# Optimization experiments

Measured on AMD Instinct MI355X. Metric: run time of the kernel, lower is better.

The kernel has to match this reference:

```python
import jax, jax.numpy as jnp
import numpy as np

S = 4            # symbol_features (number of element types)
NLAB = S * S     # label_features = 16
RC = 6.0         # cutoff radius
C1, C2 = 32, 64  # embedding_layers
B, N = 4, 512
BOX_L = 25.0     # non-periodic box extent for coordinate sampling


def setup_inputs() -> dict:
    key = jax.random.key(0)
    k1, k2, k3, k4 = jax.random.split(key, 4)
    coords = jax.random.uniform(k1, (B, N, 3), dtype=jnp.float32) * BOX_L
    numbers = jax.random.randint(k2, (B, N), 0, S)
    # NaN lattice -> Descriptor takes the non-periodic neighbor branch
    boxs = jnp.full((B, 9), jnp.nan, dtype=jnp.float32)
    # RConv parameters (per label): nuww=-0.05, sigmas=4.0, centres ~ xavier_normal
    nuww0 = jnp.full((NLAB,), -0.05, jnp.float32)
    sigmas0 = jnp.full((NLAB,), 4.0, jnp.float32)
    centres0 = (jax.random.normal(k3, (NLAB, C1)) * np.sqrt(2.0 / (NLAB + C1))).astype(jnp.float32)
    nuww1 = jnp.full((NLAB,), -0.05, jnp.float32)
    sigmas1 = jnp.full((NLAB,), 4.0, jnp.float32)
    centres1 = (jax.random.normal(k4, (NLAB, C2)) * np.sqrt(2.0 / (NLAB + C2))).astype(jnp.float32)
    return {"boxs": boxs, "numbers": numbers, "coords": coords,
            "nuww0": nuww0, "sigmas0": sigmas0, "centres0": centres0,
            "nuww1": nuww1, "sigmas1": sigmas1, "centres1": centres1}


def _rconv(label, r, nuww, sigmas, centres):
    # label: [B,N,N] int; r: [B,N,N,Cin] -> out [B,N,N,Cout]
    rs = r.sum(-1, keepdims=True)            # sum over channel dim (keepdim)
    ww = nuww[label][..., None]              # [B,N,N,1]
    sgm = sigmas[label][..., None]           # [B,N,N,1]
    cc = centres[label]                      # [B,N,N,Cout]
    alpha = (rs - cc) * sgm
    return ww * jnp.exp(-(alpha * alpha))


def reference(boxs, numbers, coords, nuww0, sigmas0, centres0, nuww1, sigmas1, centres1):
    # boxs is NaN -> non-periodic branch of Descriptor.forward.
    # Dense-mask formulation: pairs (i,j) with d<=RC, i!=j; masked entries
    # contribute exactly zero to the per-atom contractions below.
    rij = coords[:, None, :, :] - coords[:, :, None, :]      # [B,N,N,3] = x_j - x_i
    d2 = jnp.sum(rij * rij, axis=-1)                         # [B,N,N]
    safe = jnp.sqrt(jnp.where(d2 > 0, d2, 1.0))              # NaN-safe sqrt for grads
    d = jnp.where(d2 > 0, safe, 0.0)
    eye = jnp.eye(N, dtype=bool)
    mask = (jax.lax.stop_gradient(d) <= RC) & ~eye           # neighbor list (detached, as in torch)

    fc = 0.5 * jnp.cos(d * (jnp.pi / RC)) + 0.5              # cutoff_cosine, [B,N,N]
    ang = rij / safe[..., None]                              # unit direction (safe at diag)
    raij = jnp.concatenate([fc[..., None], ang * fc[..., None]], axis=-1)  # [B,N,N,4]

    label = numbers[:, :, None] * S + numbers[:, None, :]    # ZIJ_Label[z_i, z_j], [B,N,N]

    r0 = fc[..., None]                                       # rij_cos, [B,N,N,1]
    phi = _rconv(label, r0, nuww0, sigmas0, centres0)        # [B,N,N,C1]
    phi = _rconv(label, phi, nuww1, sigmas1, centres1)       # [B,N,N,C2]
    phi = phi * mask[..., None]                              # zero out non-neighbors

    # per atom i: L = phi^T @ raij over neighbors j -> [C2,4]; R = L @ L^T -> [C2,C2]
    Lm = jnp.einsum('bijc,bijf->bicf', phi, raij)            # [B,N,C2,4]
    R = jnp.einsum('bicf,bidf->bicd', Lm, Lm)                # [B,N,C2,C2]
    fro = jnp.sqrt(jnp.sum(R * R, axis=(-2, -1), keepdims=True))
    D = R / fro
    return D.reshape(B, N, C2 * C2)                          # Dij [B,N,4096]
```

## Files before the change

### kernel.cpp

```cpp
#include <hip/hip_runtime.h>
#include <math.h>

#define S_ 4
#define NLAB 16
#define C1 32
#define C2 64
#define N_ 512
#define RC 6.0f
#define PI_OVER_RC 0.5235987755982988f
#define NBMAX 96

__global__ __launch_bounds__(256, 4) void desc_kernel(
    const int* __restrict__ numbers,
    const float* __restrict__ coords,
    const float* __restrict__ nuww0, const float* __restrict__ sigmas0,
    const float* __restrict__ centres0,
    const float* __restrict__ nuww1, const float* __restrict__ sigmas1,
    const float* __restrict__ centres1,
    float* __restrict__ out)
{
    __shared__ float s_c0[NLAB * 33];
    __shared__ float s_c1[NLAB * C2];
    __shared__ float s_ww0[NLAB], s_sg0[NLAB], s_ww1[NLAB], s_sg1[NLAB];
    __shared__ float4 s_pair[4][NBMAX];
    __shared__ float  s_s1[4][NBMAX];
    __shared__ int    s_lab[4][NBMAX];
    __shared__ float4 s_Lm[4][C2];

    const int tid  = threadIdx.x;
    const int w    = tid >> 6;
    const int lane = tid & 63;
    const int bi   = blockIdx.x * 4 + w;
    const int b    = bi >> 9;
    const int i    = bi & (N_ - 1);
    const int base = b * N_;

    for (int idx = tid; idx < NLAB * C1; idx += 256) {
        int l = idx >> 5, c = idx & 31;
        s_c0[l * 33 + c] = centres0[idx];
    }
    for (int idx = tid; idx < NLAB * C2; idx += 256) s_c1[idx] = centres1[idx];
    if (tid < NLAB) {
        s_ww0[tid] = nuww0[tid]; s_sg0[tid] = sigmas0[tid];
        s_ww1[tid] = nuww1[tid]; s_sg1[tid] = sigmas1[tid];
    }
    __syncthreads();

    const float xi = coords[(base + i) * 3 + 0];
    const float yi = coords[(base + i) * 3 + 1];
    const float zi = coords[(base + i) * 3 + 2];
    const int zlab = numbers[base + i] * S_;

    int cnt = 0;
    #pragma unroll
    for (int t = 0; t < 8; ++t) {
        int j = t * 64 + lane;
        float dx = coords[(base + j) * 3 + 0] - xi;
        float dy = coords[(base + j) * 3 + 1] - yi;
        float dz = coords[(base + j) * 3 + 2] - zi;
        float d2 = dx * dx + dy * dy + dz * dz;
        float d  = sqrtf(d2);
        bool hit = (j != i) && (d <= RC);
        unsigned long long m = __ballot(hit);
        int slot = cnt + __popcll(m & ((1ull << lane) - 1ull));
        if (hit && slot < NBMAX) {
            s_pair[w][slot] = make_float4(dx, dy, dz, d);
            s_lab[w][slot]  = zlab + numbers[base + j];
        }
        cnt += __popcll(m);
    }
    const int nn = min(cnt, NBMAX);
    __builtin_amdgcn_wave_barrier();

    for (int k = lane; k < nn; k += 64) {
        float4 g  = s_pair[w][k];
        int   lab = s_lab[w][k];
        float fc  = 0.5f * __cosf(g.w * PI_OVER_RC) + 0.5f;
        float sg0 = s_sg0[lab];
        const float* c0 = &s_c0[lab * 33];
        float p0 = 0.f, p1 = 0.f;
        #pragma unroll
        for (int c = 0; c < C1; c += 2) {
            float a0 = (fc - c0[c])     * sg0;
            float a1 = (fc - c0[c + 1]) * sg0;
            p0 += __expf(-(a0 * a0));
            p1 += __expf(-(a1 * a1));
        }
        float fac = (g.w > 0.f) ? (fc / g.w) : 0.f;
        s_pair[w][k] = make_float4(fc, g.x * fac, g.y * fac, g.z * fac);
        s_s1[w][k]   = s_ww0[lab] * (p0 + p1);
    }
    __builtin_amdgcn_wave_barrier();

    float a0 = 0.f, a1 = 0.f, a2 = 0.f, a3 = 0.f;
    for (int k = 0; k < nn; ++k) {
        int    lab = s_lab[w][k];
        float  s1  = s_s1[w][k];
        float4 r4  = s_pair[w][k];
        float  al  = (s1 - s_c1[lab * C2 + lane]) * s_sg1[lab];
        float  p   = s_ww1[lab] * __expf(-(al * al));
        a0 += p * r4.x; a1 += p * r4.y; a2 += p * r4.z; a3 += p * r4.w;
    }
    s_Lm[w][lane] = make_float4(a0, a1, a2, a3);
    __builtin_amdgcn_wave_barrier();

    float g00 = a0 * a0, g01 = a0 * a1, g02 = a0 * a2, g03 = a0 * a3;
    float g11 = a1 * a1, g12 = a1 * a2, g13 = a1 * a3;
    float g22 = a2 * a2, g23 = a2 * a3, g33 = a3 * a3;
    #pragma unroll
    for (int off = 32; off >= 1; off >>= 1) {
        g00 += __shfl_xor(g00, off, 64); g01 += __shfl_xor(g01, off, 64);
        g02 += __shfl_xor(g02, off, 64); g03 += __shfl_xor(g03, off, 64);
        g11 += __shfl_xor(g11, off, 64); g12 += __shfl_xor(g12, off, 64);
        g13 += __shfl_xor(g13, off, 64); g22 += __shfl_xor(g22, off, 64);
        g23 += __shfl_xor(g23, off, 64); g33 += __shfl_xor(g33, off, 64);
    }
    float ss = g00 * g00 + g11 * g11 + g22 * g22 + g33 * g33
             + 2.f * (g01 * g01 + g02 * g02 + g03 * g03
                    + g12 * g12 + g13 * g13 + g23 * g23);
    float inv = rsqrtf(ss);

    float4 Lc0_ = s_Lm[w][(lane & 15) * 4 + 0];
    float4 Lc1_ = s_Lm[w][(lane & 15) * 4 + 1];
    float4 Lc2_ = s_Lm[w][(lane & 15) * 4 + 2];
    float4 Lc3_ = s_Lm[w][(lane & 15) * 4 + 3];
    float* po = out + (size_t)bi * (C2 * C2);
    #pragma unroll
    for (int q = 0; q < 16; ++q) {
        int dd = q * 4 + (lane >> 4);
        float4 Ld = s_Lm[w][dd];
        float4 v;
        v.x = (Lc0_.x * Ld.x + Lc0_.y * Ld.y + Lc0_.z * Ld.z + Lc0_.w * Ld.w) * inv;
        v.y = (Lc1_.x * Ld.x + Lc1_.y * Ld.y + Lc1_.z * Ld.z + Lc1_.w * Ld.w) * inv;
        v.z = (Lc2_.x * Ld.x + Lc2_.y * Ld.y + Lc2_.z * Ld.z + Lc2_.w * Ld.w) * inv;
        v.w = (Lc3_.x * Ld.x + Lc3_.y * Ld.y + Lc3_.z * Ld.z + Lc3_.w * Ld.w) * inv;
        *reinterpret_cast<float4*>(po + q * 256 + lane * 4) = v;
    }
}

extern "C" void kernel_launch(void* const* d_in, const int* in_sizes, int n_in,
                              void* d_out, int out_size, void* d_ws, size_t ws_size,
                              hipStream_t stream) {
    const int*   numbers  = (const int*)  d_in[1];
    const float* coords   = (const float*)d_in[2];
    const float* nuww0    = (const float*)d_in[3];
    const float* sigmas0  = (const float*)d_in[4];
    const float* centres0 = (const float*)d_in[5];
    const float* nuww1    = (const float*)d_in[6];
    const float* sigmas1  = (const float*)d_in[7];
    const float* centres1 = (const float*)d_in[8];
    float* out = (float*)d_out;

    const int B = in_sizes[1] / N_;
    dim3 grid(B * N_ / 4), block(256);
    desc_kernel<<<grid, block, 0, stream>>>(numbers, coords, nuww0, sigmas0,
                                            centres0, nuww1, sigmas1, centres1, out);
}
```

Measured before the change: 19.43 us.

## Split descriptor into Lm kernel and separate outer-product store kernel

After: 23.54 us. +21.2%, slower.

```diff
diff --git a/kernel.cpp b/kernel.cpp
--- a/kernel.cpp
+++ b/kernel.cpp
@@ -10,14 +10,14 @@
 #define PI_OVER_RC 0.5235987755982988f
 #define NBMAX 96
 
-__global__ __launch_bounds__(256, 4) void desc_kernel(
+__global__ __launch_bounds__(256) void lm_kernel(
     const int* __restrict__ numbers,
     const float* __restrict__ coords,
     const float* __restrict__ nuww0, const float* __restrict__ sigmas0,
     const float* __restrict__ centres0,
     const float* __restrict__ nuww1, const float* __restrict__ sigmas1,
     const float* __restrict__ centres1,
-    float* __restrict__ out)
+    float4* __restrict__ ws)
 {
     __shared__ float s_c0[NLAB * 33];
     __shared__ float s_c1[NLAB * C2];
@@ -25,7 +25,6 @@
     __shared__ float4 s_pair[4][NBMAX];
     __shared__ float  s_s1[4][NBMAX];
     __shared__ int    s_lab[4][NBMAX];
-    __shared__ float4 s_Lm[4][C2];
 
     const int tid  = threadIdx.x;
     const int w    = tid >> 6;
@@ -101,8 +100,6 @@
         float  p   = s_ww1[lab] * __expf(-(al * al));
         a0 += p * r4.x; a1 += p * r4.y; a2 += p * r4.z; a3 += p * r4.w;
     }
-    s_Lm[w][lane] = make_float4(a0, a1, a2, a3);
-    __builtin_amdgcn_wave_barrier();
 
     float g00 = a0 * a0, g01 = a0 * a1, g02 = a0 * a2, g03 = a0 * a3;
     float g11 = a1 * a1, g12 = a1 * a2, g13 = a1 * a3;
@@ -118,23 +115,34 @@
     float ss = g00 * g00 + g11 * g11 + g22 * g22 + g33 * g33
              + 2.f * (g01 * g01 + g02 * g02 + g03 * g03
                     + g12 * g12 + g13 * g13 + g23 * g23);
-    float inv = rsqrtf(ss);
+    float sqinv = sqrtf(rsqrtf(ss));
 
-    float4 Lc0_ = s_Lm[w][(lane & 15) * 4 + 0];
-    float4 Lc1_ = s_Lm[w][(lane & 15) * 4 + 1];
-    float4 Lc2_ = s_Lm[w][(lane & 15) * 4 + 2];
-    float4 Lc3_ = s_Lm[w][(lane & 15) * 4 + 3];
+    ws[bi * C2 + lane] = make_float4(a0 * sqinv, a1 * sqinv, a2 * sqinv, a3 * sqinv);
+}
+
+__global__ __launch_bounds__(256, 8) void outer_kernel(
+    const float4* __restrict__ ws,
+    float* __restrict__ out)
+{
+    __shared__ float4 sL[C2];
+    const int tid = threadIdx.x;
+    const int bi  = blockIdx.x;
+
+    if (tid < C2) sL[tid] = ws[bi * C2 + tid];
+    __syncthreads();
+
+    const int cb = (tid & 15) * 4;
+    float4 Lc0 = sL[cb + 0], Lc1 = sL[cb + 1], Lc2 = sL[cb + 2], Lc3 = sL[cb + 3];
     float* po = out + (size_t)bi * (C2 * C2);
     #pragma unroll
-    for (int q = 0; q < 16; ++q) {
-        int dd = q * 4 + (lane >> 4);
-        float4 Ld = s_Lm[w][dd];
+    for (int q = 0; q < 4; ++q) {
+        float4 Ld = sL[q * 16 + (tid >> 4)];
         float4 v;
-        v.x = (Lc0_.x * Ld.x + Lc0_.y * Ld.y + Lc0_.z * Ld.z + Lc0_.w * Ld.w) * inv;
-        v.y = (Lc1_.x * Ld.x + Lc1_.y * Ld.y + Lc1_.z * Ld.z + Lc1_.w * Ld.w) * inv;
-        v.z = (Lc2_.x * Ld.x + Lc2_.y * Ld.y + Lc2_.z * Ld.z + Lc2_.w * Ld.w) * inv;
-        v.w = (Lc3_.x * Ld.x + Lc3_.y * Ld.y + Lc3_.z * Ld.z + Lc3_.w * Ld.w) * inv;
-        *reinterpret_cast<float4*>(po + q * 256 + lane * 4) = v;
+        v.x = Lc0.x * Ld.x + Lc0.y * Ld.y + Lc0.z * Ld.z + Lc0.w * Ld.w;
+        v.y = Lc1.x * Ld.x + Lc1.y * Ld.y + Lc1.z * Ld.z + Lc1.w * Ld.w;
+        v.z = Lc2.x * Ld.x + Lc2.y * Ld.y + Lc2.z * Ld.z + Lc2.w * Ld.w;
+        v.w = Lc3.x * Ld.x + Lc3.y * Ld.y + Lc3.z * Ld.z + Lc3.w * Ld.w;
+        *reinterpret_cast<float4*>(po + q * 1024 + tid * 4) = v;
     }
 }
 
@@ -150,9 +158,10 @@
     const float* sigmas1  = (const float*)d_in[7];
     const float* centres1 = (const float*)d_in[8];
     float* out = (float*)d_out;
+    float4* ws = (float4*)d_ws;
 
     const int B = in_sizes[1] / N_;
-    dim3 grid(B * N_ / 4), block(256);
-    desc_kernel<<<grid, block, 0, stream>>>(numbers, coords, nuww0, sigmas0,
-                                            centres0, nuww1, sigmas1, centres1, out);
+    lm_kernel<<<dim3(B * N_ / 4), dim3(256), 0, stream>>>(
+        numbers, coords, nuww0, sigmas0, centres0, nuww1, sigmas1, centres1, ws);
+    outer_kernel<<<dim3(B * N_), dim3(256), 0, stream>>>(ws, out);
 }
```

## Split each atom's neighbor work across four waves with shared-memory reduction

Applied to the files above, without the earlier changes.

New measurement: 22.28 us. 14.7% more time.

```diff
diff --git a/kernel.cpp b/kernel.cpp
--- a/kernel.cpp
+++ b/kernel.cpp
@@ -8,9 +8,9 @@
 #define N_ 512
 #define RC 6.0f
 #define PI_OVER_RC 0.5235987755982988f
-#define NBMAX 96
+#define SEGCAP 32
 
-__global__ __launch_bounds__(256, 4) void desc_kernel(
+__global__ __launch_bounds__(256, 8) void desc_kernel(
     const int* __restrict__ numbers,
     const float* __restrict__ coords,
     const float* __restrict__ nuww0, const float* __restrict__ sigmas0,
@@ -22,15 +22,16 @@
     __shared__ float s_c0[NLAB * 33];
     __shared__ float s_c1[NLAB * C2];
     __shared__ float s_ww0[NLAB], s_sg0[NLAB], s_ww1[NLAB], s_sg1[NLAB];
-    __shared__ float4 s_pair[4][NBMAX];
-    __shared__ float  s_s1[4][NBMAX];
-    __shared__ int    s_lab[4][NBMAX];
-    __shared__ float4 s_Lm[4][C2];
+    __shared__ float4 s_pair[4][SEGCAP];
+    __shared__ float  s_s1[4][SEGCAP];
+    __shared__ int    s_lab[4][SEGCAP];
+    __shared__ float4 s_part[4][C2];
+    __shared__ float4 s_Lm[C2];
 
     const int tid  = threadIdx.x;
-    const int w    = tid >> 6;
+    const int wq   = tid >> 6;
     const int lane = tid & 63;
-    const int bi   = blockIdx.x * 4 + w;
+    const int bi   = blockIdx.x;
     const int b    = bi >> 9;
     const int i    = bi & (N_ - 1);
     const int base = b * N_;
@@ -51,30 +52,32 @@
     const float zi = coords[(base + i) * 3 + 2];
     const int zlab = numbers[base + i] * S_;
 
-    int cnt = 0;
+    int cntq = 0;
     #pragma unroll
-    for (int t = 0; t < 8; ++t) {
-        int j = t * 64 + lane;
+    for (int t = 0; t < 2; ++t) {
+        int j = wq * 128 + t * 64 + lane;
         float dx = coords[(base + j) * 3 + 0] - xi;
         float dy = coords[(base + j) * 3 + 1] - yi;
         float dz = coords[(base + j) * 3 + 2] - zi;
+        int   zj = numbers[base + j];
         float d2 = dx * dx + dy * dy + dz * dz;
         float d  = sqrtf(d2);
         bool hit = (j != i) && (d <= RC);
         unsigned long long m = __ballot(hit);
-        int slot = cnt + __popcll(m & ((1ull << lane) - 1ull));
-        if (hit && slot < NBMAX) {
-            s_pair[w][slot] = make_float4(dx, dy, dz, d);
-            s_lab[w][slot]  = zlab + numbers[base + j];
+        int slot = cntq + __popcll(m & ((1ull << lane) - 1ull));
+        if (hit && slot < SEGCAP) {
+            s_pair[wq][slot] = make_float4(dx, dy, dz, d);
+            s_lab[wq][slot]  = zlab + zj;
         }
-        cnt += __popcll(m);
+        cntq += __popcll(m);
     }
-    const int nn = min(cnt, NBMAX);
+    const int nnq = min(cntq, SEGCAP);
     __builtin_amdgcn_wave_barrier();
 
-    for (int k = lane; k < nn; k += 64) {
-        float4 g  = s_pair[w][k];
-        int   lab = s_lab[w][k];
+    if (lane < nnq) {
+        int   k   = lane;
+        float4 g  = s_pair[wq][k];
+        int   lab = s_lab[wq][k];
         float fc  = 0.5f * __cosf(g.w * PI_OVER_RC) + 0.5f;
         float sg0 = s_sg0[lab];
         const float* c0 = &s_c0[lab * 33];
@@ -87,22 +90,32 @@
             p1 += __expf(-(a1 * a1));
         }
         float fac = (g.w > 0.f) ? (fc / g.w) : 0.f;
-        s_pair[w][k] = make_float4(fc, g.x * fac, g.y * fac, g.z * fac);
-        s_s1[w][k]   = s_ww0[lab] * (p0 + p1);
+        s_pair[wq][k] = make_float4(fc, g.x * fac, g.y * fac, g.z * fac);
+        s_s1[wq][k]   = s_ww0[lab] * (p0 + p1);
     }
     __builtin_amdgcn_wave_barrier();
 
-    float a0 = 0.f, a1 = 0.f, a2 = 0.f, a3 = 0.f;
-    for (int k = 0; k < nn; ++k) {
-        int    lab = s_lab[w][k];
-        float  s1  = s_s1[w][k];
-        float4 r4  = s_pair[w][k];
-        float  al  = (s1 - s_c1[lab * C2 + lane]) * s_sg1[lab];
-        float  p   = s_ww1[lab] * __expf(-(al * al));
-        a0 += p * r4.x; a1 += p * r4.y; a2 += p * r4.z; a3 += p * r4.w;
+    {
+        float a0 = 0.f, a1 = 0.f, a2 = 0.f, a3 = 0.f;
+        for (int k = 0; k < nnq; ++k) {
+            int    lab = s_lab[wq][k];
+            float  s1  = s_s1[wq][k];
+            float4 r4  = s_pair[wq][k];
+            float  al  = (s1 - s_c1[lab * C2 + lane]) * s_sg1[lab];
+            float  p   = s_ww1[lab] * __expf(-(al * al));
+            a0 += p * r4.x; a1 += p * r4.y; a2 += p * r4.z; a3 += p * r4.w;
+        }
+        s_part[wq][lane] = make_float4(a0, a1, a2, a3);
     }
-    s_Lm[w][lane] = make_float4(a0, a1, a2, a3);
-    __builtin_amdgcn_wave_barrier();
+    __syncthreads();
+
+    float4 P0 = s_part[0][lane], P1 = s_part[1][lane];
+    float4 P2 = s_part[2][lane], P3 = s_part[3][lane];
+    float a0 = (P0.x + P1.x) + (P2.x + P3.x);
+    float a1 = (P0.y + P1.y) + (P2.y + P3.y);
+    float a2 = (P0.z + P1.z) + (P2.z + P3.z);
+    float a3 = (P0.w + P1.w) + (P2.w + P3.w);
+    s_Lm[lane] = make_float4(a0, a1, a2, a3);
 
     float g00 = a0 * a0, g01 = a0 * a1, g02 = a0 * a2, g03 = a0 * a3;
     float g11 = a1 * a1, g12 = a1 * a2, g13 = a1 * a3;
@@ -119,21 +132,26 @@
              + 2.f * (g01 * g01 + g02 * g02 + g03 * g03
                     + g12 * g12 + g13 * g13 + g23 * g23);
     float inv = rsqrtf(ss);
+    __builtin_amdgcn_wave_barrier();
 
-    float4 Lc0_ = s_Lm[w][(lane & 15) * 4 + 0];
-    float4 Lc1_ = s_Lm[w][(lane & 15) * 4 + 1];
-    float4 Lc2_ = s_Lm[w][(lane & 15) * 4 + 2];
-    float4 Lc3_ = s_Lm[w][(lane & 15) * 4 + 3];
+    const int cb = (lane & 15) * 4;
+    float4 Lc0 = s_Lm[cb + 0], Lc1 = s_Lm[cb + 1];
+    float4 Lc2 = s_Lm[cb + 2], Lc3 = s_Lm[cb + 3];
+    Lc0.x *= inv; Lc0.y *= inv; Lc0.z *= inv; Lc0.w *= inv;
+    Lc1.x *= inv; Lc1.y *= inv; Lc1.z *= inv; Lc1.w *= inv;
+    Lc2.x *= inv; Lc2.y *= inv; Lc2.z *= inv; Lc2.w *= inv;
+    Lc3.x *= inv; Lc3.y *= inv; Lc3.z *= inv; Lc3.w *= inv;
     float* po = out + (size_t)bi * (C2 * C2);
     #pragma unroll
-    for (int q = 0; q < 16; ++q) {
+    for (int t = 0; t < 4; ++t) {
+        int q  = wq * 4 + t;
         int dd = q * 4 + (lane >> 4);
-        float4 Ld = s_Lm[w][dd];
+        float4 Ld = s_Lm[dd];
         float4 v;
-        v.x = (Lc0_.x * Ld.x + Lc0_.y * Ld.y + Lc0_.z * Ld.z + Lc0_.w * Ld.w) * inv;
-        v.y = (Lc1_.x * Ld.x + Lc1_.y * Ld.y + Lc1_.z * Ld.z + Lc1_.w * Ld.w) * inv;
-        v.z = (Lc2_.x * Ld.x + Lc2_.y * Ld.y + Lc2_.z * Ld.z + Lc2_.w * Ld.w) * inv;
-        v.w = (Lc3_.x * Ld.x + Lc3_.y * Ld.y + Lc3_.z * Ld.z + Lc3_.w * Ld.w) * inv;
+        v.x = Lc0.x * Ld.x + Lc0.y * Ld.y + Lc0.z * Ld.z + Lc0.w * Ld.w;
+        v.y = Lc1.x * Ld.x + Lc1.y * Ld.y + Lc1.z * Ld.z + Lc1.w * Ld.w;
+        v.z = Lc2.x * Ld.x + Lc2.y * Ld.y + Lc2.z * Ld.z + Lc2.w * Ld.w;
+        v.w = Lc3.x * Ld.x + Lc3.y * Ld.y + Lc3.z * Ld.z + Lc3.w * Ld.w;
         *reinterpret_cast<float4*>(po + q * 256 + lane * 4) = v;
     }
 }
@@ -152,7 +170,7 @@
     float* out = (float*)d_out;
 
     const int B = in_sizes[1] / N_;
-    dim3 grid(B * N_ / 4), block(256);
+    dim3 grid(B * N_), block(256);
     desc_kernel<<<grid, block, 0, stream>>>(numbers, coords, nuww0, sigmas0,
                                             centres0, nuww1, sigmas1, centres1, out);
 }
```
